# Kernel tuning notes

Measured on AMD Instinct MI355X. Metric: run time of the kernel, lower is better.

## Reference

```python
import jax, jax.numpy as jnp
import numpy as np

B, H, S, D = 2, 8, 4096, 64

def setup_inputs() -> dict:
    key = jax.random.key(0)
    kq, kk, kv = jax.random.split(key, 3)
    queries = jax.random.normal(kq, (B, H, S, D), dtype=jnp.float32)
    keys = jax.random.normal(kk, (B, H, S, D), dtype=jnp.float32)
    values = jax.random.normal(kv, (B, H, S, D), dtype=jnp.float32)
    adj = jnp.zeros((1,), dtype=jnp.int32)  # unused by the module, kept for signature fidelity
    return {"queries": queries, "keys": keys, "values": values, "adj": adj}

def reference(queries, keys, values, adj):
    # scores: [B,H,S,S]; note the original divides by a hard-coded 16, not sqrt(d)
    scores = jnp.einsum('bhqd,bhkd->bhqk', queries, keys) / 16.0
    attn = jax.nn.softmax(scores, axis=-1)
    # dropout p=0.0 -> identity in eval/deterministic mode
    h = jnp.einsum('bhqk,bhkd->bhqd', attn, values)  # [B,H,S,D]
    # original uses .view (a reshape, NOT a transpose) to (S, B, H, D)
    return jnp.reshape(h, (S, B, H, D))
```

## Files before the change

kernel.cpp:

```cpp
#include <hip/hip_runtime.h>
#include <hip/hip_bf16.h>
#include <math.h>

#define S_LEN 4096
#define D_DIM 64
#define NBH   16
#define HKT   32
#define QPRE  0.09016844f

typedef __attribute__((ext_vector_type(8))) short bf16x8;
typedef __attribute__((ext_vector_type(4))) float f32x4;
typedef __attribute__((ext_vector_type(4))) __fp16 f16x4;
typedef __attribute__((ext_vector_type(2))) __fp16 f16x2;

__device__ __forceinline__ unsigned int pkbf(float lo, float hi) {
  unsigned int ua = __float_as_uint(lo) + 0x8000u;
  unsigned int ub = __float_as_uint(hi) + 0x8000u;
  return __builtin_amdgcn_perm(ub, ua, 0x07060302u);
}
__device__ __forceinline__ unsigned int pkhf(float lo, float hi) {
  f16x2 h = __builtin_amdgcn_cvt_pkrtz(lo, hi);
  return *(unsigned int*)&h;
}
__device__ __forceinline__ void dma16(const unsigned short* g, unsigned short* l) {
  __builtin_amdgcn_global_load_lds(
      (const __attribute__((address_space(1))) unsigned int*)g,
      (__attribute__((address_space(3))) unsigned int*)l, 16, 0, 0);
}

__global__ __launch_bounds__(256) void prep(const float* __restrict__ K,
                                            const float* __restrict__ V,
                                            unsigned short* __restrict__ Kbf,
                                            unsigned short* __restrict__ Vt) {
  const int tid = threadIdx.x;
  __shared__ unsigned short tile[64][72];
  if (blockIdx.x < 256) {
    const int bh = blockIdx.x >> 4, ch = blockIdx.x & 15;
    const size_t base = ((size_t)bh * S_LEN + ch * 256) * D_DIM;
#pragma unroll
    for (int p = 0; p < 8; ++p) {
      int i = tid + p * 256;
      int row = i >> 3, c = (i & 7) * 8;
      float4 a = *(const float4*)&K[base + row * D_DIM + c];
      float4 b = *(const float4*)&K[base + row * D_DIM + c + 4];
      uint4 w;
      w.x = pkbf(a.x, a.y); w.y = pkbf(a.z, a.w);
      w.z = pkbf(b.x, b.y); w.w = pkbf(b.z, b.w);
      *(uint4*)&Kbf[base + row * D_DIM + c] = w;
    }
    return;
  }
  const int blk = blockIdx.x - 256;
  const int bh = blk >> 6, kt = blk & 63;
  const float* src = V + ((size_t)bh * S_LEN + kt * 64) * D_DIM;
#pragma unroll
  for (int p = 0; p < 4; ++p) {
    int i = tid + p * 256;
    int row = i >> 4, c = (i & 15) * 4;
    float4 f = *(const float4*)&src[row * D_DIM + c];
    int cs = c ^ (((row >> 4) & 3) << 4);
    unsigned long long w = (unsigned long long)pkhf(f.x, f.y) |
                           ((unsigned long long)pkhf(f.z, f.w) << 32);
    *(unsigned long long*)&tile[row][cs] = w;
  }
  __syncthreads();
  const int kc = tid & 7;
#pragma unroll
  for (int p = 0; p < 2; ++p) {
    int d = p * 32 + (tid >> 3);
    int col = d ^ (((kc >> 1) & 3) << 4);
    union { unsigned short u[8]; uint4 v; } t;
#pragma unroll
    for (int i = 0; i < 8; ++i) t.u[i] = tile[kc * 8 + i][col];
    *(uint4*)&Vt[((size_t)bh * D_DIM + d) * S_LEN + kt * 64 + kc * 8] = t.v;
  }
}

__global__ __launch_bounds__(256, 4) void fattn(const float* __restrict__ Q,
                                                const unsigned short* __restrict__ Kbf,
                                                const unsigned short* __restrict__ Vt,
                                                unsigned short* __restrict__ Oh,
                                                float* __restrict__ Lw) {
  const int bh   = blockIdx.x & 15;
  const int qb   = (blockIdx.x >> 4) & 31;
  const int half = blockIdx.x >> 9;
  const int tid  = threadIdx.x;
  const int wave = tid >> 6;
  const int lane = tid & 63;
  const int quad = lane >> 4;
  const int l15  = lane & 15;
  const int rho  = l15 & 7;
  const int T0   = half * HKT;

  __shared__ unsigned short Ksh[2][64][64];
  __shared__ unsigned short Vsh[2][64][64];

  bf16x8 qf[2][2];
#pragma unroll
  for (int qt = 0; qt < 2; ++qt) {
    const int qg = qb * 128 + wave * 32 + qt * 16 + l15;
    const float* qp = Q + ((size_t)bh * S_LEN + qg) * D_DIM + quad * 8;
#pragma unroll
    for (int h = 0; h < 2; ++h) {
      float4 a = *(const float4*)&qp[h * 32];
      float4 b = *(const float4*)&qp[h * 32 + 4];
      union { unsigned int u[4]; bf16x8 v; } f;
      f.u[0] = pkbf(a.x * QPRE, a.y * QPRE);
      f.u[1] = pkbf(a.z * QPRE, a.w * QPRE);
      f.u[2] = pkbf(b.x * QPRE, b.y * QPRE);
      f.u[3] = pkbf(b.z * QPRE, b.w * QPRE);
      qf[qt][h] = f.v;
    }
  }

  f32x4 ot[2][4];
#pragma unroll
  for (int qt = 0; qt < 2; ++qt)
#pragma unroll
    for (int dt = 0; dt < 4; ++dt) ot[qt][dt] = (f32x4){0.f, 0.f, 0.f, 0.f};
  float Lp[2] = {0.f, 0.f};

  const unsigned short* Kb = Kbf + (size_t)bh * S_LEN * D_DIM;
  const unsigned short* Vb = Vt + (size_t)bh * D_DIM * S_LEN;

  const int r_lo = wave * 8 + (lane >> 3);
  const int csrc = ((lane & 7) ^ (lane >> 3)) * 8;

  const int ck0 = (quad ^ rho) * 8;
  const int ck1 = ((quad + 4) ^ rho) * 8;
  const int vrow  = l15 * 128 + (quad & 1) * 8;
  const int rho16 = rho << 4;
  const int vq2   = (quad >> 1) << 4;

#define DMAK(T, B) do { const int t_ = (T); \
  dma16(&Kb[(size_t)(t_ * 64 + r_lo) * 64 + csrc],      &Ksh[B][wave * 8][0]); \
  dma16(&Kb[(size_t)(t_ * 64 + r_lo + 32) * 64 + csrc], &Ksh[B][wave * 8 + 32][0]); } while (0)
#define DMAV(T, B) do { const int t_ = (T); \
  dma16(&Vb[(size_t)r_lo * S_LEN + t_ * 64 + csrc],        &Vsh[B][wave * 8][0]); \
  dma16(&Vb[(size_t)(r_lo + 32) * S_LEN + t_ * 64 + csrc], &Vsh[B][wave * 8 + 32][0]); } while (0)

#define SCORES(KB, PD) do { \
  _Pragma("unroll") \
  for (int mt = 0; mt < 4; ++mt) { \
    const int row_ = mt * 16 + l15; \
    bf16x8 kf0 = *(const bf16x8*)&Ksh[KB][row_][ck0]; \
    bf16x8 kf1 = *(const bf16x8*)&Ksh[KB][row_][ck1]; \
    _Pragma("unroll") \
    for (int qt = 0; qt < 2; ++qt) { \
      f32x4 acc = (f32x4){0.f, 0.f, 0.f, 0.f}; \
      acc = __builtin_amdgcn_mfma_f32_16x16x32_bf16(kf0, qf[qt][0], acc, 0, 0, 0); \
      acc = __builtin_amdgcn_mfma_f32_16x16x32_bf16(kf1, qf[qt][1], acc, 0, 0, 0); \
      float p0 = __builtin_amdgcn_exp2f(acc[0]); \
      float p1 = __builtin_amdgcn_exp2f(acc[1]); \
      float p2 = __builtin_amdgcn_exp2f(acc[2]); \
      float p3 = __builtin_amdgcn_exp2f(acc[3]); \
      Lp[qt] += (p0 + p1) + (p2 + p3); \
      PD[mt][qt][0] = pkhf(p0, p1); \
      PD[mt][qt][1] = pkhf(p2, p3); \
    } \
  } } while (0)

#define PVSTEP(VB, PU) do { \
  const char* vbase = (const char*)&Vsh[VB][0][0]; \
  _Pragma("unroll") \
  for (int mt = 0; mt < 4; ++mt) { \
    const int vb_ = vrow + (((mt << 5) + vq2) ^ rho16); \
    union { unsigned int u[2]; f16x4 v; } pb0, pb1; \
    pb0.u[0] = PU[mt][0][0]; pb0.u[1] = PU[mt][0][1]; \
    pb1.u[0] = PU[mt][1][0]; pb1.u[1] = PU[mt][1][1]; \
    _Pragma("unroll") \
    for (int dt = 0; dt < 4; ++dt) { \
      f16x4 va = *(const f16x4*)(vbase + vb_ + dt * 2048); \
      ot[0][dt] = __builtin_amdgcn_mfma_f32_16x16x16f16(va, pb0.v, ot[0][dt], 0, 0, 0); \
      ot[1][dt] = __builtin_amdgcn_mfma_f32_16x16x16f16(va, pb1.v, ot[1][dt], 0, 0, 0); \
    } \
  } } while (0)

#define ITER(I, KBL, KBU, VBL, VBU, PU, PD) do { \
  __syncthreads(); \
  if ((I) < HKT - 2) DMAK(T0 + (I) + 2, KBL); \
  DMAV(T0 + (I) + 1, VBL); \
  SCORES(KBU, PD); \
  PVSTEP(VBU, PU); } while (0)

  unsigned int pA[4][2][2], pB[4][2][2];

  DMAK(T0, 0); DMAV(T0, 0);
  __syncthreads();
  SCORES(0, pA);
  DMAK(T0 + 1, 1);

  for (int b = 0; b < HKT - 2; b += 2) {
    ITER(b + 0, 0, 1, 1, 0, pA, pB);
    ITER(b + 1, 1, 0, 0, 1, pB, pA);
  }
  ITER(HKT - 2, 0, 1, 1, 0, pA, pB);
  __syncthreads();
  PVSTEP(1, pB);

#pragma unroll
  for (int qt = 0; qt < 2; ++qt) {
    float Lt = Lp[qt];
    Lt += __shfl_xor(Lt, 16);
    Lt += __shfl_xor(Lt, 32);
    const size_t grow = (size_t)bh * S_LEN + qb * 128 + wave * 32 + qt * 16 + l15;
    if (quad == 0) Lw[grow * 2 + half] = Lt;
#pragma unroll
    for (int dt = 0; dt < 4; ++dt) {
      uint2 w;
      w.x = pkhf(ot[qt][dt][0], ot[qt][dt][1]);
      w.y = pkhf(ot[qt][dt][2], ot[qt][dt][3]);
      *(uint2*)&Oh[grow * 128 + half * 64 + dt * 16 + quad * 4] = w;
    }
  }
#undef DMAK
#undef DMAV
#undef SCORES
#undef PVSTEP
#undef ITER
}

__global__ __launch_bounds__(256) void reduce(unsigned short* Oh, const float* __restrict__ Lw) {
  const int tid = threadIdx.x;
  const size_t r = (size_t)blockIdx.x * 32 + (tid >> 3);
  const int d0 = (tid & 7) * 8;
  union { uint4 v; __fp16 h[8]; } a, b;
  a.v = *(const uint4*)&Oh[r * 128 + d0];
  b.v = *(const uint4*)&Oh[r * 128 + 64 + d0];
  const float linv = 1.0f / (Lw[r * 2] + Lw[r * 2 + 1]);
  float o[8];
#pragma unroll
  for (int j = 0; j < 8; ++j) o[j] = ((float)a.h[j] + (float)b.h[j]) * linv;
  __syncthreads();
  float* Of = (float*)Oh;
  float4 w0 = {o[0], o[1], o[2], o[3]};
  float4 w1 = {o[4], o[5], o[6], o[7]};
  *(float4*)&Of[r * 64 + d0]     = w0;
  *(float4*)&Of[r * 64 + d0 + 4] = w1;
}

extern "C" void kernel_launch(void* const* d_in, const int* in_sizes, int n_in,
                              void* d_out, int out_size, void* d_ws, size_t ws_size,
                              hipStream_t stream) {
  const float* Q = (const float*)d_in[0];
  const float* K = (const float*)d_in[1];
  const float* V = (const float*)d_in[2];
  unsigned short* Kbf = (unsigned short*)d_ws;
  unsigned short* Vt  = Kbf + (size_t)NBH * S_LEN * D_DIM;
  float* Lw = (float*)(Vt + (size_t)NBH * S_LEN * D_DIM);
  unsigned short* Oh = (unsigned short*)d_out;

  prep<<<1280, 256, 0, stream>>>(K, V, Kbf, Vt);
  fattn<<<NBH * 32 * 2, 256, 0, stream>>>(Q, Kbf, Vt, Oh, Lw);
  reduce<<<(NBH * S_LEN) / 32, 256, 0, stream>>>(Oh, Lw);
}
```

Baseline: 187.9 us.

## Fuse split-K reduction into attention kernel via atomic ticket; pad V LDS layout

Measured after the change: 349.5 us. 86.0% more time.

```diff
diff --git a/kernel.cpp b/kernel.cpp
--- a/kernel.cpp
+++ b/kernel.cpp
@@ -22,6 +22,11 @@
   f16x2 h = __builtin_amdgcn_cvt_pkrtz(lo, hi);
   return *(unsigned int*)&h;
 }
+__device__ __forceinline__ float dot2acc(unsigned int pk, float acc) {
+  f16x2 a = *(f16x2*)&pk;
+  const f16x2 o = {(__fp16)1.0f, (__fp16)1.0f};
+  return __builtin_amdgcn_fdot2(a, o, acc, false);
+}
 __device__ __forceinline__ void dma16(const unsigned short* g, unsigned short* l) {
   __builtin_amdgcn_global_load_lds(
       (const __attribute__((address_space(1))) unsigned int*)g,
@@ -31,10 +36,12 @@
 __global__ __launch_bounds__(256) void prep(const float* __restrict__ K,
                                             const float* __restrict__ V,
                                             unsigned short* __restrict__ Kbf,
-                                            unsigned short* __restrict__ Vt) {
+                                            unsigned short* __restrict__ Vt,
+                                            int* __restrict__ Tk) {
   const int tid = threadIdx.x;
   __shared__ unsigned short tile[64][72];
   if (blockIdx.x < 256) {
+    if (blockIdx.x == 0) { Tk[tid] = 0; Tk[tid + 256] = 0; }
     const int bh = blockIdx.x >> 4, ch = blockIdx.x & 15;
     const size_t base = ((size_t)bh * S_LEN + ch * 256) * D_DIM;
 #pragma unroll
@@ -80,7 +87,8 @@
                                                 const unsigned short* __restrict__ Kbf,
                                                 const unsigned short* __restrict__ Vt,
                                                 unsigned short* __restrict__ Oh,
-                                                float* __restrict__ Lw) {
+                                                float* __restrict__ Lw,
+                                                int* __restrict__ Tk) {
   const int bh   = blockIdx.x & 15;
   const int qb   = (blockIdx.x >> 4) & 31;
   const int half = blockIdx.x >> 9;
@@ -90,10 +98,11 @@
   const int quad = lane >> 4;
   const int l15  = lane & 15;
   const int rho  = l15 & 7;
+  const int hbit = l15 >> 3;
   const int T0   = half * HKT;
 
   __shared__ unsigned short Ksh[2][64][64];
-  __shared__ unsigned short Vsh[2][64][64];
+  __shared__ char VshRaw[2][8256];
 
   bf16x8 qf[2][2];
 #pragma unroll
@@ -128,16 +137,15 @@
 
   const int ck0 = (quad ^ rho) * 8;
   const int ck1 = ((quad + 4) ^ rho) * 8;
-  const int vrow  = l15 * 128 + (quad & 1) * 8;
-  const int rho16 = rho << 4;
-  const int vq2   = (quad >> 1) << 4;
+  const int vlane = hbit * 1032 + rho * 128 + (quad & 1) * 8;
+  const int q2v   = quad >> 1;
 
 #define DMAK(T, B) do { const int t_ = (T); \
   dma16(&Kb[(size_t)(t_ * 64 + r_lo) * 64 + csrc],      &Ksh[B][wave * 8][0]); \
   dma16(&Kb[(size_t)(t_ * 64 + r_lo + 32) * 64 + csrc], &Ksh[B][wave * 8 + 32][0]); } while (0)
 #define DMAV(T, B) do { const int t_ = (T); \
-  dma16(&Vb[(size_t)r_lo * S_LEN + t_ * 64 + csrc],        &Vsh[B][wave * 8][0]); \
-  dma16(&Vb[(size_t)(r_lo + 32) * S_LEN + t_ * 64 + csrc], &Vsh[B][wave * 8 + 32][0]); } while (0)
+  dma16(&Vb[(size_t)r_lo * S_LEN + t_ * 64 + csrc],        (unsigned short*)&VshRaw[B][(wave) * 1032]); \
+  dma16(&Vb[(size_t)(r_lo + 32) * S_LEN + t_ * 64 + csrc], (unsigned short*)&VshRaw[B][(wave + 4) * 1032]); } while (0)
 
 #define SCORES(KB, PD) do { \
   _Pragma("unroll") \
@@ -154,23 +162,24 @@
       float p1 = __builtin_amdgcn_exp2f(acc[1]); \
       float p2 = __builtin_amdgcn_exp2f(acc[2]); \
       float p3 = __builtin_amdgcn_exp2f(acc[3]); \
-      Lp[qt] += (p0 + p1) + (p2 + p3); \
       PD[mt][qt][0] = pkhf(p0, p1); \
       PD[mt][qt][1] = pkhf(p2, p3); \
+      Lp[qt] = dot2acc(PD[mt][qt][0], Lp[qt]); \
+      Lp[qt] = dot2acc(PD[mt][qt][1], Lp[qt]); \
     } \
   } } while (0)
 
 #define PVSTEP(VB, PU) do { \
-  const char* vbase = (const char*)&Vsh[VB][0][0]; \
+  const char* vraw = &VshRaw[VB][0]; \
   _Pragma("unroll") \
   for (int mt = 0; mt < 4; ++mt) { \
-    const int vb_ = vrow + (((mt << 5) + vq2) ^ rho16); \
+    const int sc16 = (((mt << 1) + q2v) ^ rho) << 4; \
     union { unsigned int u[2]; f16x4 v; } pb0, pb1; \
     pb0.u[0] = PU[mt][0][0]; pb0.u[1] = PU[mt][0][1]; \
     pb1.u[0] = PU[mt][1][0]; pb1.u[1] = PU[mt][1][1]; \
     _Pragma("unroll") \
     for (int dt = 0; dt < 4; ++dt) { \
-      f16x4 va = *(const f16x4*)(vbase + vb_ + dt * 2048); \
+      f16x4 va = *(const f16x4*)(vraw + vlane + dt * 2064 + sc16); \
       ot[0][dt] = __builtin_amdgcn_mfma_f32_16x16x16f16(va, pb0.v, ot[0][dt], 0, 0, 0); \
       ot[1][dt] = __builtin_amdgcn_mfma_f32_16x16x16f16(va, pb1.v, ot[1][dt], 0, 0, 0); \
     } \
@@ -213,30 +222,38 @@
       *(uint2*)&Oh[grow * 128 + half * 64 + dt * 16 + quad * 4] = w;
     }
   }
+
+  __shared__ int lastFlag;
+  __threadfence();
+  if (tid == 0) lastFlag = (atomicAdd(&Tk[bh * 32 + qb], 1) == 1);
+  __syncthreads();
+  if (lastFlag) {
+    __threadfence();
+    const size_t r = (size_t)bh * S_LEN + qb * 128 + (tid >> 1);
+    const int d0 = (tid & 1) * 32;
+    union { uint4 v[4]; __fp16 h[32]; } pa, pc;
+#pragma unroll
+    for (int j = 0; j < 4; ++j) {
+      pa.v[j] = *(const uint4*)&Oh[r * 128 + d0 + j * 8];
+      pc.v[j] = *(const uint4*)&Oh[r * 128 + 64 + d0 + j * 8];
+    }
+    const float linv = 1.0f / (Lw[r * 2] + Lw[r * 2 + 1]);
+    float o[32];
+#pragma unroll
+    for (int j = 0; j < 32; ++j) o[j] = ((float)pa.h[j] + (float)pc.h[j]) * linv;
+    __syncthreads();
+    float* Of = (float*)Oh;
+#pragma unroll
+    for (int j = 0; j < 8; ++j) {
+      float4 w = {o[j * 4], o[j * 4 + 1], o[j * 4 + 2], o[j * 4 + 3]};
+      *(float4*)&Of[r * 64 + d0 + j * 4] = w;
+    }
+  }
 #undef DMAK
 #undef DMAV
 #undef SCORES
 #undef PVSTEP
 #undef ITER
-}
-
-__global__ __launch_bounds__(256) void reduce(unsigned short* Oh, const float* __restrict__ Lw) {
-  const int tid = threadIdx.x;
-  const size_t r = (size_t)blockIdx.x * 32 + (tid >> 3);
-  const int d0 = (tid & 7) * 8;
-  union { uint4 v; __fp16 h[8]; } a, b;
-  a.v = *(const uint4*)&Oh[r * 128 + d0];
-  b.v = *(const uint4*)&Oh[r * 128 + 64 + d0];
-  const float linv = 1.0f / (Lw[r * 2] + Lw[r * 2 + 1]);
-  float o[8];
-#pragma unroll
-  for (int j = 0; j < 8; ++j) o[j] = ((float)a.h[j] + (float)b.h[j]) * linv;
-  __syncthreads();
-  float* Of = (float*)Oh;
-  float4 w0 = {o[0], o[1], o[2], o[3]};
-  float4 w1 = {o[4], o[5], o[6], o[7]};
-  *(float4*)&Of[r * 64 + d0]     = w0;
-  *(float4*)&Of[r * 64 + d0 + 4] = w1;
 }
 
 extern "C" void kernel_launch(void* const* d_in, const int* in_sizes, int n_in,
@@ -248,9 +265,9 @@
   unsigned short* Kbf = (unsigned short*)d_ws;
   unsigned short* Vt  = Kbf + (size_t)NBH * S_LEN * D_DIM;
   float* Lw = (float*)(Vt + (size_t)NBH * S_LEN * D_DIM);
+  int* Tk = (int*)(Lw + (size_t)2 * NBH * S_LEN);
   unsigned short* Oh = (unsigned short*)d_out;
 
-  prep<<<1280, 256, 0, stream>>>(K, V, Kbf, Vt);
-  fattn<<<NBH * 32 * 2, 256, 0, stream>>>(Q, Kbf, Vt, Oh, Lw);
-  reduce<<<(NBH * S_LEN) / 32, 256, 0, stream>>>(Oh, Lw);
-}
+  prep<<<1280, 256, 0, stream>>>(K, V, Kbf, Vt, Tk);
+  fattn<<<NBH * 32 * 2, 256, 0, stream>>>(Q, Kbf, Vt, Oh, Lw, Tk);
+}
```
